# Performance work log

Hardware: AMD Instinct MI355X
Metric: run time of the kernel (lower is better)

The kernel has to match this reference:

```python
import jax, jax.numpy as jnp
import numpy as np

B, C, H, W = 16, 256, 56, 56
HEADS = 4
C_OUT = 256
K = 3
SQ = 16  # squeeze_rate (C=256 >= 80, so not halved)
BN_EPS = 1e-5


def setup_inputs() -> dict:
    key = jax.random.key(0)
    ks = jax.random.split(key, 9)
    r = C // SQ
    cper = C_OUT // HEADS
    return {
        "x": jax.random.normal(ks[0], (B, C, H, W), dtype=jnp.float32),
        "bn_gamma": 1.0 + 0.1 * jax.random.normal(ks[1], (C,), dtype=jnp.float32),
        "bn_beta": 0.1 * jax.random.normal(ks[2], (C,), dtype=jnp.float32),
        "bn_mean": 0.1 * jax.random.normal(ks[3], (C,), dtype=jnp.float32),
        "bn_var": 0.5 + jax.random.uniform(ks[4], (C,), dtype=jnp.float32),
        "fc1_w": 0.1 * jax.random.normal(ks[5], (HEADS, r, C), dtype=jnp.float32),
        "fc2_w": 0.1 * jax.random.normal(ks[6], (HEADS, C, r), dtype=jnp.float32),
        "fc2_b": jnp.ones((HEADS, C), dtype=jnp.float32),  # init.constant_(bias, 1.0)
        "conv_w": 0.05 * jax.random.normal(ks[7], (HEADS, cper, C, K, K), dtype=jnp.float32),
        "inactive_channels": 192,
    }


def reference(x, bn_gamma, bn_beta, bn_mean, bn_var, fc1_w, fc2_w, fc2_b, conv_w, inactive_channels):
    b, c, h, w = x.shape
    heads = fc1_w.shape[0]
    # BatchNorm (inference, running stats) + ReLU
    inv = jax.lax.rsqrt(bn_var + BN_EPS)
    xn = jax.nn.relu((x - bn_mean[None, :, None, None]) * (bn_gamma * inv)[None, :, None, None]
                     + bn_beta[None, :, None, None])
    # Global average pool -> [b, c]
    x_avg = xn.mean(axis=(2, 3))
    # Per-head SE gate: relu(fc2(relu(fc1(x_avg))))  -> [heads, b, c]
    y1 = jax.nn.relu(jnp.einsum("bc,hrc->hbr", x_avg, fc1_w))
    mask = jax.nn.relu(jnp.einsum("hbr,hcr->hbc", y1, fc2_w) + fc2_b[:, None, :])
    lasso_loss = mask.mean(axis=(1, 2)).sum()  # sum over heads of per-head mean
    # topk smallest -> threshold; zero out mask values <= k-th smallest (detached cmp)
    mask_d = jax.lax.stop_gradient(mask)
    if inactive_channels > 0:
        neg_vals, _ = jax.lax.top_k(-mask_d, inactive_channels)  # k largest of -mask
        thresh = -neg_vals[..., -1:]  # k-th smallest of mask, [heads, b, 1]
        mask_c = jnp.where(mask_d <= thresh, 0.0, mask)
    else:
        mask_c = mask
    # Apply per-head channel mask and stack heads: [b, heads*c, h, w]
    mc = jnp.transpose(mask_c, (1, 0, 2))  # [b, heads, c]
    x_mask = (xn[:, None, :, :, :] * mc[:, :, :, None, None]).reshape(b, heads * c, h, w)
    # Grouped conv (groups=heads), weight [heads*cper, c, K, K]
    wflat = conv_w.reshape(-1, c, K, K)
    out = jax.lax.conv_general_dilated(
        x_mask, wflat, window_strides=(1, 1), padding=[(1, 1), (1, 1)],
        dimension_numbers=("NCHW", "OIHW", "NCHW"), feature_group_count=heads)
    bo, co, ho, wo = out.shape
    out = out.reshape(bo, heads, co // heads, ho, wo).transpose(0, 2, 1, 3, 4).reshape(bo, co, ho, wo)
    return out, lasso_loss
```

## Files before the change

kernel.cpp:

```cpp
#include <hip/hip_runtime.h>
#include <hip/hip_bf16.h>
#include <math.h>

#define B_     16
#define C_     256
#define H_     56
#define W_     56
#define HEADS_ 4
#define CPER_  64
#define R_     16
#define HW_    (H_*W_)
#define BN_EPS_ 1e-5f

typedef short bf16x8 __attribute__((ext_vector_type(8)));
typedef float f32x4  __attribute__((ext_vector_type(4)));

__device__ inline unsigned short f2bf(float f) {
    unsigned int u = __builtin_bit_cast(unsigned int, f);
    u += 0x7fffu + ((u >> 16) & 1u);
    return (unsigned short)(u >> 16);
}

__global__ __launch_bounds__(64) void k_pool(
    const float* __restrict__ x,
    const float* __restrict__ gamma, const float* __restrict__ beta,
    const float* __restrict__ mean,  const float* __restrict__ var,
    float* __restrict__ xavg)
{
    int plane = blockIdx.x;
    int c = plane & (C_ - 1);
    float s = gamma[c] * rsqrtf(var[c] + BN_EPS_);
    float t = fmaf(-mean[c], s, beta[c]);
    const float4* xp = (const float4*)(x + (size_t)plane * HW_);
    float sum = 0.f;
    for (int i = threadIdx.x; i < HW_ / 4; i += 64) {
        float4 v = xp[i];
        sum += fmaxf(fmaf(v.x, s, t), 0.f) + fmaxf(fmaf(v.y, s, t), 0.f)
             + fmaxf(fmaf(v.z, s, t), 0.f) + fmaxf(fmaf(v.w, s, t), 0.f);
    }
    for (int off = 32; off; off >>= 1) sum += __shfl_down(sum, off, 64);
    if (threadIdx.x == 0) xavg[plane] = sum * (1.f / HW_);
}

__global__ __launch_bounds__(256) void k_wt2(const float* __restrict__ w,
                                             float* __restrict__ wt2f)
{
    int i = blockIdx.x * 256 + threadIdx.x;
    if (i >= HEADS_ * 9 * CPER_ * C_) return;
    int c = i & 255, j = (i >> 8) & 63, ht = i >> 14;
    int h = ht / 9, t = ht - h * 9;
    wt2f[i] = w[((size_t)((h * CPER_ + j) * C_ + c)) * 9 + t];
}

__global__ __launch_bounds__(256) void k_se(
    const float* __restrict__ xavg,
    const float* __restrict__ fc1, const float* __restrict__ fc2,
    const float* __restrict__ fc2b, const int* __restrict__ kptr,
    float* __restrict__ maskc, int* __restrict__ aidx64,
    int* __restrict__ act_cnt, float* __restrict__ lasso)
{
    int hb = blockIdx.x;
    int h = hb / B_, b = hb - h * B_;
    int tid = threadIdx.x;

    __shared__ float sav[C_], sy1[R_], smask[C_], sred[4], sthr;
    __shared__ int scnt, s_ord[C_];

    sav[tid] = xavg[b * C_ + tid];
    if (tid == 0) scnt = 0;
    __syncthreads();

    if (tid < R_) {
        const float* w = fc1 + (size_t)(h * R_ + tid) * C_;
        float acc = 0.f;
        for (int c2 = 0; c2 < C_; ++c2) acc = fmaf(sav[c2], w[c2], acc);
        sy1[tid] = fmaxf(acc, 0.f);
    }
    __syncthreads();

    const float* w2 = fc2 + (size_t)(h * C_ + tid) * R_;
    float acc = fc2b[h * C_ + tid];
    for (int r = 0; r < R_; ++r) acc = fmaf(sy1[r], w2[r], acc);
    float m = fmaxf(acc, 0.f);
    smask[tid] = m;
    __syncthreads();

    float ls = m;
    for (int off = 32; off > 0; off >>= 1) ls += __shfl_down(ls, off, 64);
    int lane = tid & 63, wv = tid >> 6;
    if (lane == 0) sred[wv] = ls;

    int cl = 0, ce = 0;
    for (int j = 0; j < C_; ++j) {
        float vj = smask[j];
        cl += (vj < m);
        ce += (vj == m);
    }
    if (tid == 0) sthr = -1e30f;
    __syncthreads();
    int k = kptr[0];
    if (k > 0 && cl <= k - 1 && (k - 1) < cl + ce) sthr = m;
    __syncthreads();

    float thr = sthr;
    float mc = (m <= thr) ? 0.f : m;
    maskc[hb * C_ + tid] = mc;
    if (mc != 0.f) {
        int p = atomicAdd(&scnt, 1);
        s_ord[p] = tid;
    }
    __syncthreads();
    if (tid < 64) aidx64[hb * 64 + tid] = (tid < scnt) ? s_ord[tid] : 0;
    if (tid == 0) {
        act_cnt[hb] = scnt;
        atomicAdd(lasso, (sred[0] + sred[1] + sred[2] + sred[3]) * (1.f / (B_ * C_)));
    }
}

__global__ __launch_bounds__(256) void k_wgather(
    const float* __restrict__ wt2f, const float* __restrict__ maskc,
    const int* __restrict__ aidx64, const int* __restrict__ acnt,
    short* __restrict__ Wc)
{
    int t = blockIdx.x, hb = blockIdx.y;
    int h = hb >> 4;
    int tid = threadIdx.x;
    int cnt = acnt[hb];
    __shared__ int s_act[64];
    __shared__ float s_mv[64];
    if (tid < 64) {
        int a = aidx64[hb * 64 + tid];
        s_act[tid] = a;
        s_mv[tid]  = (tid < cnt) ? maskc[hb * C_ + a] : 0.f;
    }
    __syncthreads();
    const float* wsrc = wt2f + (size_t)(h * 9 + t) * (CPER_ * C_);
    short* wdst = Wc + (size_t)(hb * 9 + t) * (CPER_ * 64);
    for (int it = 0; it < 16; ++it) {
        int e = it * 256 + tid;
        int cp = e & 63, j = e >> 6;
        float v = wsrc[j * C_ + s_act[cp]] * s_mv[cp];
        int slot = (cp + 8 * (j & 7)) & 63;
        wdst[j * 64 + slot] = (short)f2bf(v);
    }
}

__global__ __launch_bounds__(256) void k_bnc(
    const float* __restrict__ x,
    const float* __restrict__ gamma, const float* __restrict__ beta,
    const float* __restrict__ mean,  const float* __restrict__ var,
    const int* __restrict__ aidx64, short* __restrict__ xc)
{
    int y = blockIdx.x, b = blockIdx.y;
    int tid = threadIdx.x;
    __shared__ unsigned short T[W_ * 258];
    __shared__ float ss[C_], st[C_];
    __shared__ short sact[256];

    {
        float s = gamma[tid] * rsqrtf(var[tid] + BN_EPS_);
        ss[tid] = s;
        st[tid] = fmaf(-mean[tid], s, beta[tid]);
        int h = tid >> 6, cp = tid & 63;
        sact[tid] = (short)aidx64[(h * B_ + b) * 64 + cp];
    }
    __syncthreads();

    const float* xrow = x + (size_t)b * C_ * HW_ + y * W_;
    for (int i = tid; i < C_ * 14; i += 256) {
        int c = i / 14, f = i - c * 14;
        float4 v = *(const float4*)(xrow + (size_t)c * HW_ + f * 4);
        float s = ss[c], t = st[c];
        int xb = f * 4;
        T[(xb + 0) * 258 + c] = f2bf(fmaxf(fmaf(v.x, s, t), 0.f));
        T[(xb + 1) * 258 + c] = f2bf(fmaxf(fmaf(v.y, s, t), 0.f));
        T[(xb + 2) * 258 + c] = f2bf(fmaxf(fmaf(v.z, s, t), 0.f));
        T[(xb + 3) * 258 + c] = f2bf(fmaxf(fmaf(v.w, s, t), 0.f));
    }
    __syncthreads();

    unsigned int* ob = (unsigned int*)xc;
    #pragma unroll
    for (int h = 0; h < HEADS_; ++h) {
        size_t obase = ((size_t)(h * B_ + b) * HW_ + (size_t)y * W_) * 32;
        for (int i = tid; i < W_ * 32; i += 256) {
            int px = i >> 5, d = i & 31;
            unsigned int lo = T[px * 258 + sact[h * 64 + 2 * d]];
            unsigned int hi = T[px * 258 + sact[h * 64 + 2 * d + 1]];
            ob[obase + i] = lo | (hi << 16);
        }
    }
}

__global__ __launch_bounds__(256, 3) void k_conv(
    const short* __restrict__ xc, const short* __restrict__ Wc,
    float* __restrict__ out)
{
    int g = blockIdx.x;
    int vx = g & 7, r = g >> 3;
    int hb = vx * 8 + r / 14;
    int band = r - (r / 14) * 14;
    int h = hb >> 4, b = hb & 15;
    int tid = threadIdx.x, lane = tid & 63, wv = tid >> 6;
    int y0 = band * 4;
    int m = lane & 15, q = lane >> 4;

    __shared__ short sW[2][4096];

    const short* Wh = Wc + (size_t)hb * 9 * 4096;
    const short* xb = xc + (size_t)hb * HW_ * 64;
    int soff = wv * 512 + lane * 8;

    {
        bf16x8 w0 = *(const bf16x8*)(Wh + soff);
        bf16x8 w1 = *(const bf16x8*)(Wh + 2048 + soff);
        *(bf16x8*)&sW[0][soff] = w0;
        *(bf16x8*)&sW[0][2048 + soff] = w1;
    }
    __syncthreads();

    f32x4 acc[4][4];
    #pragma unroll
    for (int i = 0; i < 4; ++i)
        #pragma unroll
        for (int j = 0; j < 4; ++j)
            #pragma unroll
            for (int rr = 0; rr < 4; ++rr) acc[i][j][rr] = 0.f;

    int yrow = y0 + wv;
    int arot = q * 8 + 8 * (m & 7);

    #pragma unroll
    for (int t = 0; t < 9; ++t) {
        const int dy = t / 3 - 1, dx = t % 3 - 1;
        bf16x8 w0, w1;
        if (t < 8) {
            const short* Wn = Wh + (t + 1) * 4096;
            w0 = *(const bf16x8*)(Wn + soff);
            w1 = *(const bf16x8*)(Wn + 2048 + soff);
        }
        int gy = yrow + dy;
        bool gyok = (unsigned)gy < (unsigned)H_;
        const short* sWc = sW[t & 1];

        #pragma unroll
        for (int c0 = 0; c0 < 64; c0 += 32) {
            bf16x8 aF[4], bF[4];
            #pragma unroll
            for (int jt = 0; jt < 4; ++jt)
                aF[jt] = *(const bf16x8*)&sWc[(jt * 16 + m) * 64 + ((c0 + arot) & 63)];
            #pragma unroll
            for (int xt = 0; xt < 4; ++xt) {
                int gx = xt * 16 + m + dx;
                bf16x8 v = {0, 0, 0, 0, 0, 0, 0, 0};
                if (gyok && (unsigned)gx < (unsigned)W_)
                    v = *(const bf16x8*)(xb + ((size_t)(gy * W_ + gx)) * 64 + c0 + q * 8);
                bF[xt] = v;
            }
            #pragma unroll
            for (int jt = 0; jt < 4; ++jt)
                #pragma unroll
                for (int xt = 0; xt < 4; ++xt)
                    acc[jt][xt] = __builtin_amdgcn_mfma_f32_16x16x32_bf16(
                        aF[jt], bF[xt], acc[jt][xt], 0, 0, 0);
        }
        if (t < 8) {
            *(bf16x8*)&sW[(t + 1) & 1][soff] = w0;
            *(bf16x8*)&sW[(t + 1) & 1][2048 + soff] = w1;
        }
        __syncthreads();
    }

    #pragma unroll
    for (int xt = 0; xt < 4; ++xt) {
        int xx = xt * 16 + m;
        if (xx < W_) {
            #pragma unroll
            for (int jt = 0; jt < 4; ++jt)
                #pragma unroll
                for (int rr = 0; rr < 4; ++rr) {
                    int j = jt * 16 + q * 4 + rr;
                    int oc = j * HEADS_ + h;
                    out[(((size_t)b * C_ + oc) * H_ + yrow) * W_ + xx] = acc[jt][xt][rr];
                }
        }
    }
}

extern "C" void kernel_launch(void* const* d_in, const int* in_sizes, int n_in,
                              void* d_out, int out_size, void* d_ws, size_t ws_size,
                              hipStream_t stream)
{
    const float* x     = (const float*)d_in[0];
    const float* gamma = (const float*)d_in[1];
    const float* beta  = (const float*)d_in[2];
    const float* mean  = (const float*)d_in[3];
    const float* var   = (const float*)d_in[4];
    const float* fc1   = (const float*)d_in[5];
    const float* fc2   = (const float*)d_in[6];
    const float* fc2b  = (const float*)d_in[7];
    const float* convw = (const float*)d_in[8];
    const int*   kptr  = (const int*)d_in[9];

    float* out   = (float*)d_out;
    float* lasso = out + (size_t)B_ * C_ * HW_;

    char* ws = (char*)d_ws;
    size_t off = 0;
    short* xc    = (short*)(ws + off); off += (size_t)HEADS_ * B_ * HW_ * 64 * 2;
    off = (off + 255) & ~(size_t)255;
    float* xavg  = (float*)(ws + off); off += (size_t)B_ * C_ * 4;
    float* maskc = (float*)(ws + off); off += (size_t)HEADS_ * B_ * C_ * 4;
    int*   aidx64= (int*)  (ws + off); off += (size_t)HEADS_ * B_ * 64 * 4;
    int*   acnt  = (int*)  (ws + off); off += (size_t)HEADS_ * B_ * 4;
    off = (off + 255) & ~(size_t)255;
    float* wt2f  = (float*)(ws + off); off += (size_t)HEADS_ * 9 * CPER_ * C_ * 4;
    off = (off + 255) & ~(size_t)255;
    short* Wc    = (short*)(ws + off); off += (size_t)HEADS_ * B_ * 9 * CPER_ * 64 * 2;

    hipMemsetAsync(lasso, 0, 4, stream);

    k_wt2<<<(HEADS_ * 9 * CPER_ * C_ + 255) / 256, 256, 0, stream>>>(convw, wt2f);
    k_pool<<<B_ * C_, 64, 0, stream>>>(x, gamma, beta, mean, var, xavg);
    k_se<<<HEADS_ * B_, 256, 0, stream>>>(xavg, fc1, fc2, fc2b, kptr,
                                          maskc, aidx64, acnt, lasso);
    k_wgather<<<dim3(9, HEADS_ * B_), 256, 0, stream>>>(wt2f, maskc, aidx64, acnt, Wc);
    k_bnc<<<dim3(H_, B_), 256, 0, stream>>>(x, gamma, beta, mean, var, aidx64, xc);
    k_conv<<<HEADS_ * B_ * (H_ / 4), 256, 0, stream>>>(xc, Wc, out);
}
```

Before: 194.4 us.

## Restructure BN-compact gather and stage conv weights in two bulk LDS loads

The BN+compact kernel now has each thread own one active channel and apply BN directly to it, then writes 8-byte chunks out per head. This avoids normalizing all 256 channels and the per-element shared-memory gather through index tables. The conv kernel swaps its per-tap double-buffered weight prefetch and per-tap barriers for two bulk loads into a 5-tap LDS buffer, with a single sync pair at tap 5. It also raises the occupancy hint to 4 and wraps the MFMA blocks in s_setprio. The larger LDS footprint (40KB) may cap occupancy, and the bulk reload at tap 5 stalls all waves.

Measured after the change: 191.8 us. No clear change (-1.3%).

```diff
diff --git a/kernel.cpp b/kernel.cpp
--- a/kernel.cpp
+++ b/kernel.cpp
@@ -153,46 +153,37 @@
 {
     int y = blockIdx.x, b = blockIdx.y;
     int tid = threadIdx.x;
-    __shared__ unsigned short T[W_ * 258];
-    __shared__ float ss[C_], st[C_];
-    __shared__ short sact[256];
-
-    {
-        float s = gamma[tid] * rsqrtf(var[tid] + BN_EPS_);
-        ss[tid] = s;
-        st[tid] = fmaf(-mean[tid], s, beta[tid]);
-        int h = tid >> 6, cp = tid & 63;
-        sact[tid] = (short)aidx64[(h * B_ + b) * 64 + cp];
-    }
-    __syncthreads();
-
-    const float* xrow = x + (size_t)b * C_ * HW_ + y * W_;
-    for (int i = tid; i < C_ * 14; i += 256) {
-        int c = i / 14, f = i - c * 14;
-        float4 v = *(const float4*)(xrow + (size_t)c * HW_ + f * 4);
-        float s = ss[c], t = st[c];
-        int xb = f * 4;
-        T[(xb + 0) * 258 + c] = f2bf(fmaxf(fmaf(v.x, s, t), 0.f));
-        T[(xb + 1) * 258 + c] = f2bf(fmaxf(fmaf(v.y, s, t), 0.f));
-        T[(xb + 2) * 258 + c] = f2bf(fmaxf(fmaf(v.z, s, t), 0.f));
-        T[(xb + 3) * 258 + c] = f2bf(fmaxf(fmaf(v.w, s, t), 0.f));
-    }
-    __syncthreads();
-
-    unsigned int* ob = (unsigned int*)xc;
-    #pragma unroll
-    for (int h = 0; h < HEADS_; ++h) {
-        size_t obase = ((size_t)(h * B_ + b) * HW_ + (size_t)y * W_) * 32;
-        for (int i = tid; i < W_ * 32; i += 256) {
-            int px = i >> 5, d = i & 31;
-            unsigned int lo = T[px * 258 + sact[h * 64 + 2 * d]];
-            unsigned int hi = T[px * 258 + sact[h * 64 + 2 * d + 1]];
-            ob[obase + i] = lo | (hi << 16);
-        }
-    }
-}
-
-__global__ __launch_bounds__(256, 3) void k_conv(
+    int h = tid >> 6;
+    __shared__ __align__(16) unsigned short T[W_ * 256];
+
+    int c = aidx64[(h * B_ + b) * 64 + (tid & 63)];
+    float s = gamma[c] * rsqrtf(var[c] + BN_EPS_);
+    float t0 = fmaf(-mean[c], s, beta[c]);
+    const float* xrow = x + ((size_t)(b * C_ + c)) * HW_ + y * W_;
+    #pragma unroll
+    for (int f = 0; f < 14; ++f) {
+        float4 v = *(const float4*)(xrow + f * 4);
+        int px = f * 4;
+        T[(px + 0) * 256 + tid] = f2bf(fmaxf(fmaf(v.x, s, t0), 0.f));
+        T[(px + 1) * 256 + tid] = f2bf(fmaxf(fmaf(v.y, s, t0), 0.f));
+        T[(px + 2) * 256 + tid] = f2bf(fmaxf(fmaf(v.z, s, t0), 0.f));
+        T[(px + 3) * 256 + tid] = f2bf(fmaxf(fmaf(v.w, s, t0), 0.f));
+    }
+    __syncthreads();
+
+    const uint2* Ts = (const uint2*)T;
+    uint2* ob = (uint2*)xc;
+    #pragma unroll
+    for (int it = 0; it < 14; ++it) {
+        int e = it * 256 + tid;
+        int px = e >> 6, col4 = e & 63;
+        int hh = col4 >> 4, cp4 = col4 & 15;
+        uint2 v = Ts[px * 64 + col4];
+        ob[((size_t)(hh * B_ + b) * HW_ + (size_t)y * W_ + px) * 16 + cp4] = v;
+    }
+}
+
+__global__ __launch_bounds__(256, 4) void k_conv(
     const short* __restrict__ xc, const short* __restrict__ Wc,
     float* __restrict__ out)
 {
@@ -205,17 +196,15 @@
     int y0 = band * 4;
     int m = lane & 15, q = lane >> 4;
 
-    __shared__ short sW[2][4096];
+    __shared__ short sW[5 * 4096];
 
     const short* Wh = Wc + (size_t)hb * 9 * 4096;
     const short* xb = xc + (size_t)hb * HW_ * 64;
-    int soff = wv * 512 + lane * 8;
-
-    {
-        bf16x8 w0 = *(const bf16x8*)(Wh + soff);
-        bf16x8 w1 = *(const bf16x8*)(Wh + 2048 + soff);
-        *(bf16x8*)&sW[0][soff] = w0;
-        *(bf16x8*)&sW[0][2048 + soff] = w1;
+
+    #pragma unroll
+    for (int it = 0; it < 10; ++it) {
+        int e = it * 256 + tid;
+        *(bf16x8*)&sW[e * 8] = *(const bf16x8*)(Wh + e * 8);
     }
     __syncthreads();
 
@@ -232,16 +221,19 @@
 
     #pragma unroll
     for (int t = 0; t < 9; ++t) {
+        if (t == 5) {
+            __syncthreads();
+            #pragma unroll
+            for (int it = 0; it < 8; ++it) {
+                int e = it * 256 + tid;
+                *(bf16x8*)&sW[e * 8] = *(const bf16x8*)(Wh + 20480 + e * 8);
+            }
+            __syncthreads();
+        }
         const int dy = t / 3 - 1, dx = t % 3 - 1;
-        bf16x8 w0, w1;
-        if (t < 8) {
-            const short* Wn = Wh + (t + 1) * 4096;
-            w0 = *(const bf16x8*)(Wn + soff);
-            w1 = *(const bf16x8*)(Wn + 2048 + soff);
-        }
         int gy = yrow + dy;
         bool gyok = (unsigned)gy < (unsigned)H_;
-        const short* sWc = sW[t & 1];
+        const short* sWc = sW + (t < 5 ? t : t - 5) * 4096;
 
         #pragma unroll
         for (int c0 = 0; c0 < 64; c0 += 32) {
@@ -257,18 +249,15 @@
                     v = *(const bf16x8*)(xb + ((size_t)(gy * W_ + gx)) * 64 + c0 + q * 8);
                 bF[xt] = v;
             }
+            __builtin_amdgcn_s_setprio(1);
             #pragma unroll
             for (int jt = 0; jt < 4; ++jt)
                 #pragma unroll
                 for (int xt = 0; xt < 4; ++xt)
                     acc[jt][xt] = __builtin_amdgcn_mfma_f32_16x16x32_bf16(
                         aF[jt], bF[xt], acc[jt][xt], 0, 0, 0);
+            __builtin_amdgcn_s_setprio(0);
         }
-        if (t < 8) {
-            *(bf16x8*)&sW[(t + 1) & 1][soff] = w0;
-            *(bf16x8*)&sW[(t + 1) & 1][2048 + soff] = w1;
-        }
-        __syncthreads();
     }
 
     #pragma unroll
```
